# Optimization experiments

Hardware: AMD Instinct MI355X
Metric: run time of the kernel (lower is better)

## Reference

```python
import jax, jax.numpy as jnp
import numpy as np

NEG_SLOPE = 0.2  # PyG GATConv leaky_relu slope


def _embed(feats, W1, b1, W2, b2, Wc, bc):
    # collapse_esm (two plain Linears, no activation) then linear_comb
    esm = feats[..., 24:] @ W1 + b1
    esm = esm @ W2 + b2
    x = jnp.concatenate([feats[..., :24], esm], axis=-1)
    return x @ Wc + bc


def _gat_conv(x, src, dst, n, W, a_src, a_dst, b, concat):
    # PyG GATConv: project, per-edge attention logits, softmax over incoming edges at dst,
    # weighted scatter-sum. Self loops already included in (src, dst).
    H, C = a_src.shape
    h = (x @ W).reshape(-1, H, C)                 # [N,H,C]
    s = (h * a_src).sum(-1)                       # [N,H]
    d = (h * a_dst).sum(-1)                       # [N,H]
    e = jax.nn.leaky_relu(s[src] + d[dst], NEG_SLOPE)  # [E,H]
    m = jax.ops.segment_max(e, dst, num_segments=n)
    e = jnp.exp(e - m[dst])
    z = jax.ops.segment_sum(e, dst, num_segments=n)
    alpha = e / z[dst]                            # [E,H]
    out = jax.ops.segment_sum(h[src] * alpha[:, :, None], dst, num_segments=n)  # [N,H,C]
    out = out.reshape(n, H * C) if concat else out.mean(axis=1)
    return out + b


def setup_inputs() -> dict:
    key = jax.random.key(0)
    ks = jax.random.split(key, 24)
    N, E, B, F = 100000, 3200000, 8, 50
    NF, M1, M2, M3, CH = 1304, 652, 326, 350, 32
    L, H, HID = 3, 8, 4
    f32 = jnp.float32
    inp = {
        "node_features": jax.random.normal(ks[0], (N, NF), f32),
        "edge_index": jax.random.randint(ks[1], (2, E), 0, N, dtype=jnp.int32),
        "edge_attr": jax.random.normal(ks[2], (E, 8), f32),
        "frag_emb": jax.random.normal(ks[3], (B, F, NF), f32),
        "W_esm1": jax.random.normal(ks[4], (NF - 24, M1), f32) / np.sqrt(NF - 24),
        "b_esm1": jnp.zeros((M1,), f32),
        "W_esm2": jax.random.normal(ks[5], (M1, M2), f32) / np.sqrt(M1),
        "b_esm2": jnp.zeros((M2,), f32),
        "W_comb": jax.random.normal(ks[6], (M3, CH), f32) / np.sqrt(M3),
        "b_comb": jnp.zeros((CH,), f32),
        "gat1_W": jax.random.normal(ks[7], (L, CH, H * HID), f32) / np.sqrt(CH),
        "gat1_asrc": jax.random.normal(ks[8], (L, H, HID), f32) * 0.1,
        "gat1_adst": jax.random.normal(ks[9], (L, H, HID), f32) * 0.1,
        "gat1_b": jnp.zeros((L, H * HID), f32),
        "gat2_W": jax.random.normal(ks[10], (L, H * HID, CH), f32) / np.sqrt(H * HID),
        "gat2_asrc": jax.random.normal(ks[11], (L, 1, CH), f32) * 0.1,
        "gat2_adst": jax.random.normal(ks[12], (L, 1, CH), f32) * 0.1,
        "gat2_b": jnp.zeros((L, CH), f32),
        "W_fin": jax.random.normal(ks[13], (CH, 1), f32) / np.sqrt(CH),
        "b_fin": jnp.zeros((1,), f32),
    }
    return inp


def reference(node_features, edge_index, edge_attr, frag_emb,
              W_esm1, b_esm1, W_esm2, b_esm2, W_comb, b_comb,
              gat1_W, gat1_asrc, gat1_adst, gat1_b,
              gat2_W, gat2_asrc, gat2_adst, gat2_b,
              W_fin, b_fin):
    N = node_features.shape[0]
    loop = jnp.arange(N, dtype=edge_index.dtype)
    src = jnp.concatenate([edge_index[0], loop])  # self loops (PyG default)
    dst = jnp.concatenate([edge_index[1], loop])

    x = _embed(node_features, W_esm1, b_esm1, W_esm2, b_esm2, W_comb, b_comb)  # [N,32]
    for i in range(gat1_W.shape[0]):
        x = _gat_conv(x, src, dst, N, gat1_W[i], gat1_asrc[i], gat1_adst[i], gat1_b[i], True)
        x = jax.nn.elu(x)
        x = _gat_conv(x, src, dst, N, gat2_W[i], gat2_asrc[i], gat2_adst[i], gat2_b[i], False)

    ys = _embed(frag_emb, W_esm1, b_esm1, W_esm2, b_esm2, W_comb, b_comb)  # [B,F,32]
    B, F, C = ys.shape
    xb = x.reshape(B, N // B, C)                      # equal-size graphs
    A = jax.nn.softmax(jnp.einsum('bnd,bfd->bnf', xb, ys), axis=-1)
    p = jnp.einsum('bnf,bfd->bnd', A, ys)             # [B,n,32]
    return jax.nn.sigmoid(p @ W_fin + b_fin).squeeze(-1)  # [B,n]
```

## Files before the change

### kernel.cpp

```cpp
#include <hip/hip_runtime.h>
#include <hip/hip_bf16.h>

#define NF 1304
#define M1 652
#define M2 326
#define CH 32
#define NHEAD1 8
#define HID1 4
#define NLAYER 3
#define FRAG 50
#define NBATCH 8
#define DPAD 16

static inline int ceil_div(int a, int b){ return (a + b - 1)/b; }

__device__ __forceinline__ unsigned short f2bf(float f){
  unsigned u = __float_as_uint(f);
  unsigned r = ((u >> 16) & 1u) + 0x7fffu;
  return (unsigned short)((u + r) >> 16);
}
__device__ __forceinline__ float bf2f(unsigned short b){
  return __uint_as_float(((unsigned)b) << 16);
}

#define TM 64
#define TN 64
#define TKK 16
__global__ __launch_bounds__(256) void gemm_bias(
    const float* __restrict__ A, int lda,
    const float* __restrict__ B, int ldb,
    const float* __restrict__ bias,
    float* __restrict__ C, int ldc,
    int M, int N, int K, int acc)
{
  __shared__ float As[TKK][TM + 1];
  __shared__ float Bs[TKK][TN];
  int tid = threadIdx.x;
  int tx = tid & 15, ty = tid >> 4;
  int row0 = blockIdx.y * TM, col0 = blockIdx.x * TN;
  float c[4][4] = {};
  for (int k0 = 0; k0 < K; k0 += TKK) {
    #pragma unroll
    for (int p = 0; p < 4; ++p) {
      int r = (tid >> 4) + p * 16;
      int kk = tid & 15;
      int gr = row0 + r, gk = k0 + kk;
      float v = 0.f;
      if (gr < M && gk < K) v = A[(long long)gr * lda + gk];
      As[kk][r] = v;
    }
    #pragma unroll
    for (int p = 0; p < 4; ++p) {
      int kk = (tid >> 6) + p * 4;
      int cc = tid & 63;
      int gk = k0 + kk, gc = col0 + cc;
      float v = 0.f;
      if (gk < K && gc < N) v = B[(long long)gk * ldb + gc];
      Bs[kk][cc] = v;
    }
    __syncthreads();
    #pragma unroll
    for (int kk = 0; kk < TKK; ++kk) {
      float a[4], b[4];
      #pragma unroll
      for (int i = 0; i < 4; ++i) a[i] = As[kk][ty + 16 * i];
      #pragma unroll
      for (int j = 0; j < 4; ++j) b[j] = Bs[kk][tx + 16 * j];
      #pragma unroll
      for (int i = 0; i < 4; ++i)
        #pragma unroll
        for (int j = 0; j < 4; ++j)
          c[i][j] += a[i] * b[j];
    }
    __syncthreads();
  }
  #pragma unroll
  for (int i = 0; i < 4; ++i) {
    int gr = row0 + ty + 16 * i;
    if (gr >= M) continue;
    #pragma unroll
    for (int j = 0; j < 4; ++j) {
      int gc = col0 + tx + 16 * j;
      if (gc >= N) continue;
      float v = c[i][j];
      if (bias) v += bias[gc];
      if (acc) v += C[(long long)gr * ldc + gc];
      C[(long long)gr * ldc + gc] = v;
    }
  }
}

__global__ void fold_misc_kernel(const float* __restrict__ Wc, const float* __restrict__ T1,
                                 const float* __restrict__ b1, const float* __restrict__ b2,
                                 const float* __restrict__ bc,
                                 float* __restrict__ Wbig, float* __restrict__ bfold)
{
  int tid = threadIdx.x;
  for (int i = tid; i < 24 * CH; i += 256) Wbig[i] = Wc[i];
  if (tid < CH) {
    float v = bc[tid];
    for (int k = 0; k < M2; ++k) v += b2[k] * Wc[(24 + k) * CH + tid];
    for (int i = 0; i < M1; ++i) v += b1[i] * T1[i * CH + tid];
    bfold[tid] = v;
  }
}

#define EK 64
__global__ __launch_bounds__(256) void gemm_n32(
    const float* __restrict__ A, int M, int K,
    const float* __restrict__ W, const float* __restrict__ bias,
    float* __restrict__ C)
{
  __shared__ float As[64][65];
  __shared__ float Ws[EK][32];
  int tid = threadIdx.x;
  int row0 = blockIdx.x * 64;
  int tx = tid & 7, ty = tid >> 3;
  float c0[4] = {}, c1[4] = {};
  for (int k0 = 0; k0 < K; k0 += EK) {
    #pragma unroll
    for (int p = 0; p < 4; ++p) {
      int q = tid + p * 256;
      int r = q >> 4, c4 = (q & 15) * 4;
      int gr = row0 + r, gk = k0 + c4;
      float4 v = make_float4(0.f, 0.f, 0.f, 0.f);
      if (gr < M) {
        if (gk + 3 < K) v = *(const float4*)&A[(long long)gr * K + gk];
        else {
          float t[4] = {0.f, 0.f, 0.f, 0.f};
          for (int i = 0; i < 4; ++i) if (gk + i < K) t[i] = A[(long long)gr * K + gk + i];
          v = make_float4(t[0], t[1], t[2], t[3]);
        }
      }
      As[r][c4 + 0] = v.x; As[r][c4 + 1] = v.y; As[r][c4 + 2] = v.z; As[r][c4 + 3] = v.w;
    }
    #pragma unroll
    for (int p = 0; p < 2; ++p) {
      int q = tid + p * 256;
      int r = q >> 3, c4 = (q & 7) * 4;
      int gk = k0 + r;
      float4 v = make_float4(0.f, 0.f, 0.f, 0.f);
      if (gk < K) v = *(const float4*)&W[(long long)gk * 32 + c4];
      *(float4*)&Ws[r][c4] = v;
    }
    __syncthreads();
    #pragma unroll
    for (int kk = 0; kk < EK; ++kk) {
      float4 b = *(const float4*)&Ws[kk][tx * 4];
      float a0 = As[ty * 2][kk], a1 = As[ty * 2 + 1][kk];
      c0[0] += a0 * b.x; c0[1] += a0 * b.y; c0[2] += a0 * b.z; c0[3] += a0 * b.w;
      c1[0] += a1 * b.x; c1[1] += a1 * b.y; c1[2] += a1 * b.z; c1[3] += a1 * b.w;
    }
    __syncthreads();
  }
  float4 bb = *(const float4*)&bias[tx * 4];
  int gr0 = row0 + ty * 2;
  if (gr0 < M) {
    float4 v = make_float4(c0[0] + bb.x, c0[1] + bb.y, c0[2] + bb.z, c0[3] + bb.w);
    *(float4*)&C[(long long)gr0 * 32 + tx * 4] = v;
  }
  if (gr0 + 1 < M) {
    float4 v = make_float4(c1[0] + bb.x, c1[1] + bb.y, c1[2] + bb.z, c1[3] + bb.w);
    *(float4*)&C[(long long)(gr0 + 1) * 32 + tx * 4] = v;
  }
}

__global__ void zero_deg_kernel(int* __restrict__ degp, long long n)
{
  long long i = (long long)blockIdx.x * 256 + threadIdx.x;
  if (i < n) degp[i] = 0;
}
__global__ void rank_kernel(const int* __restrict__ ei, int E,
                            int* __restrict__ degp, int* __restrict__ rank)
{
  int e = blockIdx.x * 256 + threadIdx.x;
  if (e < E) rank[e] = atomicAdd(&degp[(long long)ei[E + e] * DPAD], 1);
}
__global__ void partial_kernel(const int* __restrict__ degp, int N, int* __restrict__ partial)
{
  __shared__ int sd[256];
  int i = blockIdx.x * 256 + threadIdx.x;
  sd[threadIdx.x] = (i < N) ? degp[(long long)i * DPAD] : 0;
  __syncthreads();
  for (int off = 128; off > 0; off >>= 1) {
    if (threadIdx.x < off) sd[threadIdx.x] += sd[threadIdx.x + off];
    __syncthreads();
  }
  if (threadIdx.x == 0) partial[blockIdx.x] = sd[0];
}
__global__ void scanp_kernel(int* __restrict__ partial, int NB)
{
  __shared__ int sd[512];
  int t = threadIdx.x;
  int v = (t < NB) ? partial[t] : 0;
  sd[t] = v;
  __syncthreads();
  for (int off = 1; off < 512; off <<= 1) {
    int u = (t >= off) ? sd[t - off] : 0;
    __syncthreads();
    sd[t] += u;
    __syncthreads();
  }
  if (t < NB) partial[t] = sd[t] - v;
}
__global__ void scan_final_kernel(const int* __restrict__ degp, int N,
                                  const int* __restrict__ partial,
                                  int* __restrict__ rowptr)
{
  __shared__ int sd[256];
  int i = blockIdx.x * 256 + threadIdx.x;
  int t = threadIdx.x;
  int v = (i < N) ? degp[(long long)i * DPAD] : 0;
  sd[t] = v;
  __syncthreads();
  for (int off = 1; off < 256; off <<= 1) {
    int u = (t >= off) ? sd[t - off] : 0;
    __syncthreads();
    sd[t] += u;
    __syncthreads();
  }
  if (i < N) {
    int excl = partial[blockIdx.x] + sd[t] - v;
    rowptr[i] = excl;
    if (i == N - 1) rowptr[N] = excl + v;
  }
}
__global__ void scatter_plain_kernel(const int* __restrict__ ei, int E,
                                     const int* __restrict__ rowptr,
                                     const int* __restrict__ rank,
                                     int* __restrict__ csr)
{
  int e = blockIdx.x * 256 + threadIdx.x;
  if (e >= E) return;
  int dn = ei[E + e];
  csr[rowptr[dn] + rank[e]] = ei[e];
}

template<int H, int C>
__global__ __launch_bounds__(256) void proj_sd_kernel(
    const float* __restrict__ x, const float* __restrict__ W,
    const float* __restrict__ asrc, const float* __restrict__ adst,
    unsigned short* __restrict__ h, float* __restrict__ sv, float* __restrict__ dv, int N)
{
  __shared__ float Ws[CH][CH];
  __shared__ float al[2][CH];
  int tid = threadIdx.x;
  for (int i = tid; i < CH * CH; i += 256) Ws[i >> 5][i & 31] = W[i];
  if (tid < CH) { al[0][tid] = asrc[tid]; al[1][tid] = adst[tid]; }
  __syncthreads();
  int n = blockIdx.x * 256 + tid;
  if (n >= N) return;
  float xr[CH];
  #pragma unroll
  for (int j = 0; j < CH / 4; ++j) {
    float4 v = *(const float4*)&x[(long long)n * CH + j * 4];
    xr[j * 4] = v.x; xr[j * 4 + 1] = v.y; xr[j * 4 + 2] = v.z; xr[j * 4 + 3] = v.w;
  }
  float hr[CH] = {};
  #pragma unroll
  for (int c = 0; c < CH; ++c) {
    float xc = xr[c];
    #pragma unroll
    for (int j4 = 0; j4 < CH / 4; ++j4) {
      float4 w = *(const float4*)&Ws[c][j4 * 4];
      hr[j4 * 4] += xc * w.x; hr[j4 * 4 + 1] += xc * w.y;
      hr[j4 * 4 + 2] += xc * w.z; hr[j4 * 4 + 3] += xc * w.w;
    }
  }
  unsigned pk[16];
  #pragma unroll
  for (int j = 0; j < 16; ++j)
    pk[j] = (unsigned)f2bf(hr[2 * j]) | ((unsigned)f2bf(hr[2 * j + 1]) << 16);
  uint4* hp = (uint4*)&h[(long long)n * 32];
  #pragma unroll
  for (int j = 0; j < 4; ++j)
    hp[j] = make_uint4(pk[4 * j], pk[4 * j + 1], pk[4 * j + 2], pk[4 * j + 3]);
  #pragma unroll
  for (int hh = 0; hh < H; ++hh) {
    float ss = 0.f, dd = 0.f;
    #pragma unroll
    for (int c = 0; c < C; ++c) {
      float v = hr[hh * C + c];
      ss += v * al[0][hh * C + c];
      dd += v * al[1][hh * C + c];
    }
    sv[(long long)n * H + hh] = ss;
    dv[(long long)n * H + hh] = dd;
  }
}

template<int H, int C>
__global__ __launch_bounds__(256) void gat_gather_kernel(
    const int* __restrict__ rowptr, const int* __restrict__ csr,
    const float* __restrict__ sv, const float* __restrict__ dv,
    const unsigned* __restrict__ hp, const float* __restrict__ bias,
    float* __restrict__ xout, int N, int do_elu)
{
  int wid = threadIdx.x >> 6;
  int lane = threadIdx.x & 63;
  int n = blockIdx.x * 4 + wid;
  if (n >= N) return;
  int cpair = lane & 15;
  int slot = lane >> 4;
  int hh = (C == HID1) ? (cpair >> 1) : 0;
  float dn = dv[(long long)n * H + hh];
  float acc0 = 0.f, acc1 = 0.f, z = 0.f;
  if (slot == 0) {
    float lg = sv[(long long)n * H + hh] + dn;
    lg = lg > 0.f ? lg : 0.2f * lg;
    float w = expf(lg);
    z = w;
    unsigned u = hp[(long long)n * 16 + cpair];
    acc0 = w * bf2f((unsigned short)(u & 0xffff));
    acc1 = w * bf2f((unsigned short)(u >> 16));
  }
  int start = rowptr[n], end = rowptr[n + 1];
  for (int base = start; base < end; base += 64) {
    int m = end - base; if (m > 64) m = 64;
    int idx = (base + lane < end) ? csr[base + lane] : 0;
    int k = slot;
    for (; k + 4 < m; k += 8) {
      int si0 = __shfl(idx, k, 64);
      int si1 = __shfl(idx, k + 4, 64);
      float s0 = sv[(long long)si0 * H + hh];
      float s1 = sv[(long long)si1 * H + hh];
      unsigned u0 = hp[(long long)si0 * 16 + cpair];
      unsigned u1 = hp[(long long)si1 * 16 + cpair];
      float lg0 = s0 + dn; lg0 = lg0 > 0.f ? lg0 : 0.2f * lg0;
      float lg1 = s1 + dn; lg1 = lg1 > 0.f ? lg1 : 0.2f * lg1;
      float w0 = expf(lg0);
      float w1 = expf(lg1);
      z += w0 + w1;
      acc0 += w0 * bf2f((unsigned short)(u0 & 0xffff)) + w1 * bf2f((unsigned short)(u1 & 0xffff));
      acc1 += w0 * bf2f((unsigned short)(u0 >> 16)) + w1 * bf2f((unsigned short)(u1 >> 16));
    }
    if (k < m) {
      int si0 = __shfl(idx, k, 64);
      float s0 = sv[(long long)si0 * H + hh];
      unsigned u0 = hp[(long long)si0 * 16 + cpair];
      float lg0 = s0 + dn; lg0 = lg0 > 0.f ? lg0 : 0.2f * lg0;
      float w0 = expf(lg0);
      z += w0;
      acc0 += w0 * bf2f((unsigned short)(u0 & 0xffff));
      acc1 += w0 * bf2f((unsigned short)(u0 >> 16));
    }
  }
  acc0 += __shfl_xor(acc0, 16, 64); acc0 += __shfl_xor(acc0, 32, 64);
  acc1 += __shfl_xor(acc1, 16, 64); acc1 += __shfl_xor(acc1, 32, 64);
  z    += __shfl_xor(z, 16, 64);    z    += __shfl_xor(z, 32, 64);
  if (slot == 0) {
    int ch = cpair * 2;
    float v0 = acc0 / z + bias[ch];
    float v1 = acc1 / z + bias[ch + 1];
    if (do_elu) {
      v0 = v0 > 0.f ? v0 : (expf(v0) - 1.f);
      v1 = v1 > 0.f ? v1 : (expf(v1) - 1.f);
    }
    *(float2*)&xout[(long long)n * 32 + ch] = make_float2(v0, v1);
  }
}

__global__ __launch_bounds__(256) void pool_kernel(
    const float* __restrict__ x, const float* __restrict__ ys,
    const float* __restrict__ Wfin, const float* __restrict__ bfin,
    float* __restrict__ out, int NB)
{
  __shared__ float ysl[FRAG][CH];
  __shared__ float tl[FRAG];
  int b = blockIdx.y;
  int tid = threadIdx.x;
  for (int idx = tid; idx < FRAG * CH; idx += 256)
    ysl[idx >> 5][idx & 31] = ys[(long long)b * FRAG * CH + idx];
  __syncthreads();
  if (tid < FRAG) {
    float t = 0.f;
    #pragma unroll
    for (int dd = 0; dd < CH; ++dd) t += ysl[tid][dd] * Wfin[dd];
    tl[tid] = t;
  }
  __syncthreads();
  int n = blockIdx.x * 256 + tid;
  if (n >= NB) return;
  const float* xr = x + ((long long)b * NB + n) * CH;
  float xreg[CH];
  #pragma unroll
  for (int dd = 0; dd < CH; ++dd) xreg[dd] = xr[dd];
  float mx = -1e30f;
  for (int f = 0; f < FRAG; ++f) {
    float l = 0.f;
    #pragma unroll
    for (int dd = 0; dd < CH; ++dd) l += xreg[dd] * ysl[f][dd];
    mx = fmaxf(mx, l);
  }
  float se = 0.f, sw = 0.f;
  for (int f = 0; f < FRAG; ++f) {
    float l = 0.f;
    #pragma unroll
    for (int dd = 0; dd < CH; ++dd) l += xreg[dd] * ysl[f][dd];
    float e = expf(l - mx);
    se += e; sw += e * tl[f];
  }
  float logit = sw / se + bfin[0];
  out[(long long)b * NB + n] = 1.f / (1.f + expf(-logit));
}

extern "C" void kernel_launch(void* const* d_in, const int* in_sizes, int n_in,
                              void* d_out, int out_size, void* d_ws, size_t ws_size,
                              hipStream_t stream)
{
  const float* feats = (const float*)d_in[0];
  const int*   ei    = (const int*)d_in[1];
  const float* frag  = (const float*)d_in[3];
  const float* W1    = (const float*)d_in[4];
  const float* b1    = (const float*)d_in[5];
  const float* W2    = (const float*)d_in[6];
  const float* b2    = (const float*)d_in[7];
  const float* Wc    = (const float*)d_in[8];
  const float* bc    = (const float*)d_in[9];
  const float* g1W   = (const float*)d_in[10];
  const float* g1as  = (const float*)d_in[11];
  const float* g1ad  = (const float*)d_in[12];
  const float* g1b   = (const float*)d_in[13];
  const float* g2W   = (const float*)d_in[14];
  const float* g2as  = (const float*)d_in[15];
  const float* g2ad  = (const float*)d_in[16];
  const float* g2b   = (const float*)d_in[17];
  const float* Wfin  = (const float*)d_in[18];
  const float* bfin  = (const float*)d_in[19];

  const int N  = in_sizes[0] / NF;
  const int E  = in_sizes[1] / 2;
  const int BF = in_sizes[3] / NF;
  const int NB = N / NBATCH;

  char* ws = (char*)d_ws;
  size_t off = 0;
  auto walloc = [&](size_t bytes) -> void* {
    void* p = ws + off;
    off += (bytes + 255) & ~(size_t)255;
    return p;
  };
  float* T1     = (float*)walloc((size_t)M1 * CH * 4);
  float* Wbig   = (float*)walloc((size_t)NF * CH * 4);
  float* bfold  = (float*)walloc((size_t)CH * 4);
  float* x0     = (float*)walloc((size_t)N * CH * 4);
  float* x1     = (float*)walloc((size_t)N * CH * 4);
  unsigned short* hbuf = (unsigned short*)walloc((size_t)N * CH * 2);
  float* sbuf   = (float*)walloc((size_t)N * NHEAD1 * 4);
  float* dbuf   = (float*)walloc((size_t)N * NHEAD1 * 4);
  float* ysb    = (float*)walloc((size_t)BF * CH * 4);
  int*   degp   = (int*)walloc((size_t)N * DPAD * 4);
  int*   rowptr = (int*)walloc((size_t)(N + 1) * 4);
  int*   rank   = (int*)walloc((size_t)E * 4);
  int*   part   = (int*)walloc((size_t)512 * 4);
  int*   csr    = (int*)walloc((size_t)E * 4);
  (void)ws_size; (void)n_in; (void)out_size;

  {
    dim3 g1(1, ceil_div(M1, TM));
    gemm_bias<<<g1, 256, 0, stream>>>(W2, M2, Wc + 24 * CH, CH, nullptr, T1, CH,
                                      M1, CH, M2, 0);
    dim3 g2(1, ceil_div(NF - 24, TM));
    gemm_bias<<<g2, 256, 0, stream>>>(W1, M1, T1, CH, nullptr, Wbig + 24 * CH, CH,
                                      NF - 24, CH, M1, 0);
    fold_misc_kernel<<<1, 256, 0, stream>>>(Wc, T1, b1, b2, bc, Wbig, bfold);
  }

  {
    long long npad = (long long)N * DPAD;
    int nb = ceil_div(N, 256);
    zero_deg_kernel<<<(int)((npad + 255) / 256), 256, 0, stream>>>(degp, npad);
    rank_kernel<<<ceil_div(E, 256), 256, 0, stream>>>(ei, E, degp, rank);
    partial_kernel<<<nb, 256, 0, stream>>>(degp, N, part);
    scanp_kernel<<<1, 512, 0, stream>>>(part, nb);
    scan_final_kernel<<<nb, 256, 0, stream>>>(degp, N, part, rowptr);
    scatter_plain_kernel<<<ceil_div(E, 256), 256, 0, stream>>>(ei, E, rowptr, rank, csr);
  }

  gemm_n32<<<ceil_div(N, 64), 256, 0, stream>>>(feats, N, NF, Wbig, bfold, x0);
  gemm_n32<<<ceil_div(BF, 64), 256, 0, stream>>>(frag, BF, NF, Wbig, bfold, ysb);

  auto conv = [&](const float* xin, float* xout, const float* W, const float* as_,
                  const float* ad_, const float* bias, int H, int do_elu) {
    if (H == NHEAD1) {
      proj_sd_kernel<NHEAD1, HID1><<<ceil_div(N, 256), 256, 0, stream>>>(
          xin, W, as_, ad_, hbuf, sbuf, dbuf, N);
      gat_gather_kernel<NHEAD1, HID1><<<ceil_div(N, 4), 256, 0, stream>>>(
          rowptr, csr, sbuf, dbuf, (const unsigned*)hbuf, bias, xout, N, do_elu);
    } else {
      proj_sd_kernel<1, CH><<<ceil_div(N, 256), 256, 0, stream>>>(
          xin, W, as_, ad_, hbuf, sbuf, dbuf, N);
      gat_gather_kernel<1, CH><<<ceil_div(N, 4), 256, 0, stream>>>(
          rowptr, csr, sbuf, dbuf, (const unsigned*)hbuf, bias, xout, N, do_elu);
    }
  };

  for (int l = 0; l < NLAYER; ++l) {
    conv(x0, x1, g1W + l * CH * CH, g1as + l * NHEAD1 * HID1, g1ad + l * NHEAD1 * HID1,
         g1b + l * CH, NHEAD1, 1);
    conv(x1, x0, g2W + l * CH * CH, g2as + l * CH, g2ad + l * CH,
         g2b + l * CH, 1, 0);
  }

  pool_kernel<<<dim3(ceil_div(NB, 256), NBATCH), 256, 0, stream>>>(
      x0, ysb, Wfin, bfin, (float*)d_out, NB);
}
```

Baseline: 1.350 ms.

## Pack source features and logits into one record; unroll gather four-way

Puts the bf16 projected features and the per-head source attention logits into one interleaved 128-byte record per node, so each gathered neighbour needs a single record instead of two separate arrays. The gather loop is unrolled to four neighbours per slot to keep more loads in flight. DPAD also grows from 16 to 32, which doubles the degree scratch buffer. The cost is a larger per-node footprint: the record is padded to 32 words while only 24 are used.

```diff
diff --git a/kernel.cpp b/kernel.cpp
--- a/kernel.cpp
+++ b/kernel.cpp
@@ -10,7 +10,8 @@
 #define NLAYER 3
 #define FRAG 50
 #define NBATCH 8
-#define DPAD 16
+#define DPAD 32
+#define RSTR 32
 
 static inline int ceil_div(int a, int b){ return (a + b - 1)/b; }
 
@@ -240,7 +241,7 @@
 __global__ __launch_bounds__(256) void proj_sd_kernel(
     const float* __restrict__ x, const float* __restrict__ W,
     const float* __restrict__ asrc, const float* __restrict__ adst,
-    unsigned short* __restrict__ h, float* __restrict__ sv, float* __restrict__ dv, int N)
+    unsigned* __restrict__ rec, float* __restrict__ dv, int N)
 {
   __shared__ float Ws[CH][CH];
   __shared__ float al[2][CH];
@@ -267,14 +268,15 @@
       hr[j4 * 4 + 2] += xc * w.z; hr[j4 * 4 + 3] += xc * w.w;
     }
   }
+  unsigned* rp = rec + (long long)n * RSTR;
   unsigned pk[16];
   #pragma unroll
   for (int j = 0; j < 16; ++j)
     pk[j] = (unsigned)f2bf(hr[2 * j]) | ((unsigned)f2bf(hr[2 * j + 1]) << 16);
-  uint4* hp = (uint4*)&h[(long long)n * 32];
   #pragma unroll
   for (int j = 0; j < 4; ++j)
-    hp[j] = make_uint4(pk[4 * j], pk[4 * j + 1], pk[4 * j + 2], pk[4 * j + 3]);
+    ((uint4*)rp)[j] = make_uint4(pk[4 * j], pk[4 * j + 1], pk[4 * j + 2], pk[4 * j + 3]);
+  float sv4[H], dv4[H];
   #pragma unroll
   for (int hh = 0; hh < H; ++hh) {
     float ss = 0.f, dd = 0.f;
@@ -284,16 +286,20 @@
       ss += v * al[0][hh * C + c];
       dd += v * al[1][hh * C + c];
     }
-    sv[(long long)n * H + hh] = ss;
-    dv[(long long)n * H + hh] = dd;
+    sv4[hh] = ss; dv4[hh] = dd;
+  }
+  #pragma unroll
+  for (int hh = 0; hh < H; ++hh) {
+    rp[16 + hh] = __float_as_uint(sv4[hh]);
+    dv[(long long)n * H + hh] = dv4[hh];
   }
 }
 
 template<int H, int C>
 __global__ __launch_bounds__(256) void gat_gather_kernel(
     const int* __restrict__ rowptr, const int* __restrict__ csr,
-    const float* __restrict__ sv, const float* __restrict__ dv,
-    const unsigned* __restrict__ hp, const float* __restrict__ bias,
+    const unsigned* __restrict__ rec, const float* __restrict__ dv,
+    const float* __restrict__ bias,
     float* __restrict__ xout, int N, int do_elu)
 {
   int wid = threadIdx.x >> 6;
@@ -306,11 +312,12 @@
   float dn = dv[(long long)n * H + hh];
   float acc0 = 0.f, acc1 = 0.f, z = 0.f;
   if (slot == 0) {
-    float lg = sv[(long long)n * H + hh] + dn;
+    const unsigned* rp = rec + (long long)n * RSTR;
+    float lg = __uint_as_float(rp[16 + hh]) + dn;
     lg = lg > 0.f ? lg : 0.2f * lg;
     float w = expf(lg);
     z = w;
-    unsigned u = hp[(long long)n * 16 + cpair];
+    unsigned u = rp[cpair];
     acc0 = w * bf2f((unsigned short)(u & 0xffff));
     acc1 = w * bf2f((unsigned short)(u >> 16));
   }
@@ -319,25 +326,38 @@
     int m = end - base; if (m > 64) m = 64;
     int idx = (base + lane < end) ? csr[base + lane] : 0;
     int k = slot;
-    for (; k + 4 < m; k += 8) {
+    for (; k + 12 < m; k += 16) {
       int si0 = __shfl(idx, k, 64);
       int si1 = __shfl(idx, k + 4, 64);
-      float s0 = sv[(long long)si0 * H + hh];
-      float s1 = sv[(long long)si1 * H + hh];
-      unsigned u0 = hp[(long long)si0 * 16 + cpair];
-      unsigned u1 = hp[(long long)si1 * 16 + cpair];
+      int si2 = __shfl(idx, k + 8, 64);
+      int si3 = __shfl(idx, k + 12, 64);
+      const unsigned* r0 = rec + (long long)si0 * RSTR;
+      const unsigned* r1 = rec + (long long)si1 * RSTR;
+      const unsigned* r2 = rec + (long long)si2 * RSTR;
+      const unsigned* r3 = rec + (long long)si3 * RSTR;
+      unsigned u0 = r0[cpair]; float s0 = __uint_as_float(r0[16 + hh]);
+      unsigned u1 = r1[cpair]; float s1 = __uint_as_float(r1[16 + hh]);
+      unsigned u2 = r2[cpair]; float s2 = __uint_as_float(r2[16 + hh]);
+      unsigned u3 = r3[cpair]; float s3 = __uint_as_float(r3[16 + hh]);
       float lg0 = s0 + dn; lg0 = lg0 > 0.f ? lg0 : 0.2f * lg0;
       float lg1 = s1 + dn; lg1 = lg1 > 0.f ? lg1 : 0.2f * lg1;
-      float w0 = expf(lg0);
-      float w1 = expf(lg1);
-      z += w0 + w1;
-      acc0 += w0 * bf2f((unsigned short)(u0 & 0xffff)) + w1 * bf2f((unsigned short)(u1 & 0xffff));
-      acc1 += w0 * bf2f((unsigned short)(u0 >> 16)) + w1 * bf2f((unsigned short)(u1 >> 16));
-    }
-    if (k < m) {
+      float lg2 = s2 + dn; lg2 = lg2 > 0.f ? lg2 : 0.2f * lg2;
+      float lg3 = s3 + dn; lg3 = lg3 > 0.f ? lg3 : 0.2f * lg3;
+      float w0 = expf(lg0), w1 = expf(lg1), w2 = expf(lg2), w3 = expf(lg3);
+      z += (w0 + w1) + (w2 + w3);
+      acc0 += w0 * bf2f((unsigned short)(u0 & 0xffff))
+            + w1 * bf2f((unsigned short)(u1 & 0xffff))
+            + w2 * bf2f((unsigned short)(u2 & 0xffff))
+            + w3 * bf2f((unsigned short)(u3 & 0xffff));
+      acc1 += w0 * bf2f((unsigned short)(u0 >> 16))
+            + w1 * bf2f((unsigned short)(u1 >> 16))
+            + w2 * bf2f((unsigned short)(u2 >> 16))
+            + w3 * bf2f((unsigned short)(u3 >> 16));
+    }
+    for (; k < m; k += 4) {
       int si0 = __shfl(idx, k, 64);
-      float s0 = sv[(long long)si0 * H + hh];
-      unsigned u0 = hp[(long long)si0 * 16 + cpair];
+      const unsigned* r0 = rec + (long long)si0 * RSTR;
+      unsigned u0 = r0[cpair]; float s0 = __uint_as_float(r0[16 + hh]);
       float lg0 = s0 + dn; lg0 = lg0 > 0.f ? lg0 : 0.2f * lg0;
       float w0 = expf(lg0);
       z += w0;
@@ -440,20 +460,19 @@
     off += (bytes + 255) & ~(size_t)255;
     return p;
   };
-  float* T1     = (float*)walloc((size_t)M1 * CH * 4);
-  float* Wbig   = (float*)walloc((size_t)NF * CH * 4);
-  float* bfold  = (float*)walloc((size_t)CH * 4);
-  float* x0     = (float*)walloc((size_t)N * CH * 4);
-  float* x1     = (float*)walloc((size_t)N * CH * 4);
-  unsigned short* hbuf = (unsigned short*)walloc((size_t)N * CH * 2);
-  float* sbuf   = (float*)walloc((size_t)N * NHEAD1 * 4);
-  float* dbuf   = (float*)walloc((size_t)N * NHEAD1 * 4);
-  float* ysb    = (float*)walloc((size_t)BF * CH * 4);
-  int*   degp   = (int*)walloc((size_t)N * DPAD * 4);
-  int*   rowptr = (int*)walloc((size_t)(N + 1) * 4);
-  int*   rank   = (int*)walloc((size_t)E * 4);
-  int*   part   = (int*)walloc((size_t)512 * 4);
-  int*   csr    = (int*)walloc((size_t)E * 4);
+  float*    T1     = (float*)walloc((size_t)M1 * CH * 4);
+  float*    Wbig   = (float*)walloc((size_t)NF * CH * 4);
+  float*    bfold  = (float*)walloc((size_t)CH * 4);
+  float*    x0     = (float*)walloc((size_t)N * CH * 4);
+  float*    x1     = (float*)walloc((size_t)N * CH * 4);
+  unsigned* rec    = (unsigned*)walloc((size_t)N * RSTR * 4);
+  float*    dbuf   = (float*)walloc((size_t)N * NHEAD1 * 4);
+  float*    ysb    = (float*)walloc((size_t)BF * CH * 4);
+  int*      degp   = (int*)walloc((size_t)N * DPAD * 4);
+  int*      rowptr = (int*)walloc((size_t)(N + 1) * 4);
+  int*      rank   = (int*)walloc((size_t)E * 4);
+  int*      part   = (int*)walloc((size_t)512 * 4);
+  int*      csr    = (int*)walloc((size_t)E * 4);
   (void)ws_size; (void)n_in; (void)out_size;
 
   {
@@ -484,14 +503,14 @@
                   const float* ad_, const float* bias, int H, int do_elu) {
     if (H == NHEAD1) {
       proj_sd_kernel<NHEAD1, HID1><<<ceil_div(N, 256), 256, 0, stream>>>(
-          xin, W, as_, ad_, hbuf, sbuf, dbuf, N);
+          xin, W, as_, ad_, rec, dbuf, N);
       gat_gather_kernel<NHEAD1, HID1><<<ceil_div(N, 4), 256, 0, stream>>>(
-          rowptr, csr, sbuf, dbuf, (const unsigned*)hbuf, bias, xout, N, do_elu);
+          rowptr, csr, rec, dbuf, bias, xout, N, do_elu);
     } else {
       proj_sd_kernel<1, CH><<<ceil_div(N, 256), 256, 0, stream>>>(
-          xin, W, as_, ad_, hbuf, sbuf, dbuf, N);
+          xin, W, as_, ad_, rec, dbuf, N);
       gat_gather_kernel<1, CH><<<ceil_div(N, 4), 256, 0, stream>>>(
-          rowptr, csr, sbuf, dbuf, (const unsigned*)hbuf, bias, xout, N, do_elu);
+          rowptr, csr, rec, dbuf, bias, xout, N, do_elu);
     }
   };
 
```

New measurement: 1.348 ms. No clear change (-0.2%).
